# Optimization experiments

Hardware: AMD Instinct MI355X
Metric: run time of the kernel (lower is better)

The kernel has to match this reference:

```python
import jax, jax.numpy as jnp
import numpy as np

# Constructor constants (WindowCCC defaults)
STRIDE = 1
MAX_STRIDE = 125      # 25 * 5
WINDOW = 500          # 25 * 20


def setup_inputs() -> dict:
    key = jax.random.key(0)
    k1, k2 = jax.random.split(key)
    L = 16384000  # 32768 windows of 500
    return {
        "prediction": jax.random.normal(k1, (L,), dtype=jnp.float32),
        "ground_truth": jax.random.normal(k2, (L,), dtype=jnp.float32),
    }


def _suffix_sum(x):
    # suffix_sum[:, n] = sum_{i>=n} x[:, i]
    return jnp.cumsum(x[:, ::-1], axis=1)[:, ::-1]


def reference(prediction, ground_truth):
    # NOTE on faithfulness: in the torch source, `pred` is reassigned inside the
    # shift loop (drop first n, pad n zeros on top). Because shift indices are
    # strictly increasing (range(0, maxStride, stride)), the cumulative effect at
    # step n is exactly pred_n = [zeros(n), pred_orig[n:]]. We exploit that, and
    # express the per-shift mean/var/cov as suffix sums gathered at the shift
    # offsets -- one fused pass instead of O(num_wins * n_shifts) tiny kernels.
    W = WINDOW
    L = ground_truth.shape[0]
    num_wins = L // W
    g = ground_truth[: num_wins * W].reshape(num_wins, W)
    p = prediction[: num_wins * W].reshape(num_wins, W)

    shifts = jnp.arange(0, MAX_STRIDE, STRIDE)  # [S]
    Wf = jnp.asarray(W, p.dtype)

    # ground-truth stats (shift-independent), torch.var is unbiased (ddof=1)
    m_g = jnp.mean(g, axis=1, keepdims=True)                         # [nw,1]
    var_g = jnp.sum((g - m_g) ** 2, axis=1, keepdims=True) / (W - 1)  # [nw,1]

    # shifted-prediction stats via suffix sums, gathered at shift offsets
    Sp = _suffix_sum(p)[:, shifts]        # sum p_i, i>=n        [nw,S]
    Spp = _suffix_sum(p * p)[:, shifts]   # sum p_i^2, i>=n      [nw,S]
    Spg = _suffix_sum(p * g)[:, shifts]   # sum p_i g_i, i>=n    [nw,S]

    m_p = Sp / Wf                                   # mean of zero-padded pred_n
    var_p = (Spp - Wf * m_p * m_p) / (W - 1)        # unbiased var of pred_n
    cov = Spg / Wf - m_p * m_g                      # biased cov (torch.mean)

    denom = var_g + var_p + (m_g - m_p) ** 2
    ccc = 2.0 * cov / denom                          # [nw,S]

    cmin = jnp.min(ccc, axis=1)                      # [nw]
    return 1.0 - jnp.mean(cmin)
```

## Files before the change

kernel.cpp:

```cpp
#include <hip/hip_runtime.h>
#include <float.h>

#define WINDOW  500
#define NQUADS  125
#define NSHIFT  125
#define WPB     4

template <int CTRL, int RM>
__device__ __forceinline__ float dpp_add_step(float x) {
    int t = __builtin_amdgcn_update_dpp(0, __float_as_int(x), CTRL, RM, 0xf, false);
    return x + __int_as_float(t);
}
__device__ __forceinline__ float scan64_add(float x) {
    x = dpp_add_step<0x111, 0xf>(x);
    x = dpp_add_step<0x112, 0xf>(x);
    x = dpp_add_step<0x114, 0xf>(x);
    x = dpp_add_step<0x118, 0xf>(x);
    x = dpp_add_step<0x142, 0xa>(x);
    x = dpp_add_step<0x143, 0xc>(x);
    return x;
}
template <int CTRL, int RM>
__device__ __forceinline__ float dpp_min_step(float x) {
    int t = __builtin_amdgcn_update_dpp(0x7f800000 , __float_as_int(x),
                                        CTRL, RM, 0xf, false);
    return fminf(x, __int_as_float(t));
}
__device__ __forceinline__ float wave_min64(float x) {
    x = dpp_min_step<0x111, 0xf>(x);
    x = dpp_min_step<0x112, 0xf>(x);
    x = dpp_min_step<0x114, 0xf>(x);
    x = dpp_min_step<0x118, 0xf>(x);
    x = dpp_min_step<0x142, 0xa>(x);
    x = dpp_min_step<0x143, 0xc>(x);
    return __int_as_float(__builtin_amdgcn_readlane(__float_as_int(x), 63));
}
__device__ __forceinline__ float rl63(float x) {
    return __int_as_float(__builtin_amdgcn_readlane(__float_as_int(x), 63));
}
__device__ __forceinline__ float frcp(float x) {
    float r = __builtin_amdgcn_rcpf(x);
    return r * (2.0f - x * r);
}

__device__ __forceinline__ float ccc_eval(float Sp, float Spp, float Spg,
                                          float m_g, float var_g) {
    const float invW   = 1.0f / (float)WINDOW;
    const float invWm1 = 1.0f / (float)(WINDOW - 1);
    float m_p   = Sp * invW;
    float var_p = (Spp - (float)WINDOW * m_p * m_p) * invWm1;
    float cov   = Spg * invW - m_p * m_g;
    float d     = m_g - m_p;
    return 2.0f * cov * frcp(var_g + var_p + d * d);
}

template <bool TWO_STAGE>
__global__ __launch_bounds__(256) void window_ccc_kernel(
    const float4* __restrict__ pred4,
    const float4* __restrict__ gt4,
    float* __restrict__ block_out,
    int num_wins)
{
    __shared__ float s_cmin[WPB];
    const int wave = threadIdx.x >> 6;
    const int lane = threadIdx.x & 63;
    int w = blockIdx.x * WPB + wave;
    const bool valid = (w < num_wins);
    if (!valid) w = num_wins - 1;

    const float4* p4 = pred4 + (size_t)w * NQUADS;
    const float4* g4 = gt4   + (size_t)w * NQUADS;

    float4 pa = p4[lane];
    float4 ga = g4[lane];
    float4 pb = make_float4(0.f, 0.f, 0.f, 0.f);
    float4 gb = make_float4(0.f, 0.f, 0.f, 0.f);
    if (lane < NQUADS - 64) { pb = p4[64 + lane]; gb = g4[64 + lane]; }

    const float qp  = pa.x + pa.y + pa.z + pa.w;
    const float qpp = pa.x*pa.x + pa.y*pa.y + pa.z*pa.z + pa.w*pa.w;
    const float qpg = pa.x*ga.x + pa.y*ga.y + pa.z*ga.z + pa.w*ga.w;
    const float r1p  = pb.x + pb.y + pb.z + pb.w;
    const float r1pp = pb.x*pb.x + pb.y*pb.y + pb.z*pb.z + pb.w*pb.w;
    const float r1pg = pb.x*gb.x + pb.y*gb.y + pb.z*gb.z + pb.w*gb.w;
    const float lg  = ga.x + ga.y + ga.z + ga.w + gb.x + gb.y + gb.z + gb.w;
    const float lgg = ga.x*ga.x + ga.y*ga.y + ga.z*ga.z + ga.w*ga.w
                    + gb.x*gb.x + gb.y*gb.y + gb.z*gb.z + gb.w*gb.w;

    float c_p  = scan64_add(qp);
    float c_pp = scan64_add(qpp);
    float c_pg = scan64_add(qpg);
    float t1p  = scan64_add(r1p);
    float t1pp = scan64_add(r1pp);
    float t1pg = scan64_add(r1pg);
    float tg   = scan64_add(lg);
    float tgg  = scan64_add(lgg);

    const float sp  = rl63(c_p)  + rl63(t1p);
    const float spp = rl63(c_pp) + rl63(t1pp);
    const float spg = rl63(c_pg) + rl63(t1pg);
    const float sg  = rl63(tg);
    const float sgg = rl63(tgg);

    const float invW   = 1.0f / (float)WINDOW;
    const float invWm1 = 1.0f / (float)(WINDOW - 1);
    const float m_g   = sg * invW;
    const float var_g = (sgg - (float)WINDOW * m_g * m_g) * invWm1;

    float cmin = FLT_MAX;
    if (lane < 32) {
        float Sp  = sp  - (c_p  - qp);
        float Spp = spp - (c_pp - qpp);
        float Spg = spg - (c_pg - qpg);
        const int base = lane * 4;
        cmin = ccc_eval(Sp, Spp, Spg, m_g, var_g);
        Sp -= pa.x; Spp -= pa.x*pa.x; Spg -= pa.x*ga.x;
        if (base + 1 < NSHIFT) cmin = fminf(cmin, ccc_eval(Sp, Spp, Spg, m_g, var_g));
        Sp -= pa.y; Spp -= pa.y*pa.y; Spg -= pa.y*ga.y;
        if (base + 2 < NSHIFT) cmin = fminf(cmin, ccc_eval(Sp, Spp, Spg, m_g, var_g));
        Sp -= pa.z; Spp -= pa.z*pa.z; Spg -= pa.z*ga.z;
        if (base + 3 < NSHIFT) cmin = fminf(cmin, ccc_eval(Sp, Spp, Spg, m_g, var_g));
    }

    const float cm = wave_min64(cmin);

    if (lane == 0) s_cmin[wave] = valid ? cm : 0.f;
    __syncthreads();
    if (threadIdx.x == 0) {
        float s = s_cmin[0] + s_cmin[1] + s_cmin[2] + s_cmin[3];
        if (TWO_STAGE) block_out[blockIdx.x] = s;
        else           atomicAdd(block_out, s);
    }
}

__global__ __launch_bounds__(256) void window_ccc_finalize(
    const float* __restrict__ block_sums, int nblocks,
    float* __restrict__ out, int num_wins)
{
    float s = 0.f;
    for (int i = threadIdx.x; i < nblocks; i += 256) s += block_sums[i];
    #pragma unroll
    for (int off = 32; off >= 1; off >>= 1) s += __shfl_xor(s, off);
    __shared__ float ws[4];
    const int wave = threadIdx.x >> 6, lane = threadIdx.x & 63;
    if (lane == 0) ws[wave] = s;
    __syncthreads();
    if (threadIdx.x == 0)
        out[0] = 1.0f - (ws[0] + ws[1] + ws[2] + ws[3]) / (float)num_wins;
}

extern "C" void kernel_launch(void* const* d_in, const int* in_sizes, int n_in,
                              void* d_out, int out_size, void* d_ws, size_t ws_size,
                              hipStream_t stream) {
    const float4* pred4 = (const float4*)d_in[0];
    const float4* gt4   = (const float4*)d_in[1];
    float* out = (float*)d_out;
    float* ws  = (float*)d_ws;

    const int L = in_sizes[0];
    const int num_wins = L / WINDOW;
    const int nblocks  = (num_wins + WPB - 1) / WPB;

    if (ws_size >= (size_t)nblocks * sizeof(float)) {
        window_ccc_kernel<true><<<nblocks, 256, 0, stream>>>(pred4, gt4, ws, num_wins);
        window_ccc_finalize<<<1, 256, 0, stream>>>(ws, nblocks, out, num_wins);
    } else {
        hipMemsetAsync(ws, 0, sizeof(float), stream);
        window_ccc_kernel<false><<<nblocks, 256, 0, stream>>>(pred4, gt4, ws, num_wins);
        window_ccc_finalize<<<1, 256, 0, stream>>>(ws, 1, out, num_wins);
    }
}
```

Measured before the change: 34.23 us.

## Process four windows per wave with double-buffered register prefetch

Each wave now handles four windows strided across the grid instead of one, and the grid is cut by four. Loads for the next window are issued into a second register buffer before the current window is computed, so memory latency overlaps with the scans and CCC evaluation. A launch-bounds occupancy hint is added, and block partial sums and finalize work shrink. The trade-offs are higher register pressure and fewer blocks (2048) to fill the GPU.

```diff
diff --git a/kernel.cpp b/kernel.cpp
--- a/kernel.cpp
+++ b/kernel.cpp
@@ -5,6 +5,7 @@
 #define NQUADS  125
 #define NSHIFT  125
 #define WPB     4
+#define NWPW    4
 
 template <int CTRL, int RM>
 __device__ __forceinline__ float dpp_add_step(float x) {
@@ -22,8 +23,7 @@
 }
 template <int CTRL, int RM>
 __device__ __forceinline__ float dpp_min_step(float x) {
-    int t = __builtin_amdgcn_update_dpp(0x7f800000 , __float_as_int(x),
-                                        CTRL, RM, 0xf, false);
+    int t = __builtin_amdgcn_update_dpp(0x7f800000, __float_as_int(x), CTRL, RM, 0xf, false);
     return fminf(x, __int_as_float(t));
 }
 __device__ __forceinline__ float wave_min64(float x) {
@@ -54,28 +54,24 @@
     return 2.0f * cov * frcp(var_g + var_p + d * d);
 }
 
-template <bool TWO_STAGE>
-__global__ __launch_bounds__(256) void window_ccc_kernel(
-    const float4* __restrict__ pred4,
-    const float4* __restrict__ gt4,
-    float* __restrict__ block_out,
-    int num_wins)
+struct Win { float4 pa, ga, pb, gb; };
+
+__device__ __forceinline__ void load_win(const float4* __restrict__ pred4,
+                                         const float4* __restrict__ gt4,
+                                         int w, int lane, Win& d)
 {
-    __shared__ float s_cmin[WPB];
-    const int wave = threadIdx.x >> 6;
-    const int lane = threadIdx.x & 63;
-    int w = blockIdx.x * WPB + wave;
-    const bool valid = (w < num_wins);
-    if (!valid) w = num_wins - 1;
-
     const float4* p4 = pred4 + (size_t)w * NQUADS;
     const float4* g4 = gt4   + (size_t)w * NQUADS;
+    d.pa = p4[lane];
+    d.ga = g4[lane];
+    d.pb = make_float4(0.f, 0.f, 0.f, 0.f);
+    d.gb = make_float4(0.f, 0.f, 0.f, 0.f);
+    if (lane < NQUADS - 64) { d.pb = p4[64 + lane]; d.gb = g4[64 + lane]; }
+}
 
-    float4 pa = p4[lane];
-    float4 ga = g4[lane];
-    float4 pb = make_float4(0.f, 0.f, 0.f, 0.f);
-    float4 gb = make_float4(0.f, 0.f, 0.f, 0.f);
-    if (lane < NQUADS - 64) { pb = p4[64 + lane]; gb = g4[64 + lane]; }
+__device__ __forceinline__ float compute_win(const Win& d, int lane)
+{
+    const float4 pa = d.pa, ga = d.ga, pb = d.pb, gb = d.gb;
 
     const float qp  = pa.x + pa.y + pa.z + pa.w;
     const float qpp = pa.x*pa.x + pa.y*pa.y + pa.z*pa.z + pa.w*pa.w;
@@ -90,17 +86,11 @@
     float c_p  = scan64_add(qp);
     float c_pp = scan64_add(qpp);
     float c_pg = scan64_add(qpg);
-    float t1p  = scan64_add(r1p);
-    float t1pp = scan64_add(r1pp);
-    float t1pg = scan64_add(r1pg);
-    float tg   = scan64_add(lg);
-    float tgg  = scan64_add(lgg);
-
-    const float sp  = rl63(c_p)  + rl63(t1p);
-    const float spp = rl63(c_pp) + rl63(t1pp);
-    const float spg = rl63(c_pg) + rl63(t1pg);
-    const float sg  = rl63(tg);
-    const float sgg = rl63(tgg);
+    const float sp  = rl63(c_p)  + rl63(scan64_add(r1p));
+    const float spp = rl63(c_pp) + rl63(scan64_add(r1pp));
+    const float spg = rl63(c_pg) + rl63(scan64_add(r1pg));
+    const float sg  = rl63(scan64_add(lg));
+    const float sgg = rl63(scan64_add(lgg));
 
     const float invW   = 1.0f / (float)WINDOW;
     const float invWm1 = 1.0f / (float)(WINDOW - 1);
@@ -121,13 +111,45 @@
         Sp -= pa.z; Spp -= pa.z*pa.z; Spg -= pa.z*ga.z;
         if (base + 3 < NSHIFT) cmin = fminf(cmin, ccc_eval(Sp, Spp, Spg, m_g, var_g));
     }
+    return wave_min64(cmin);
+}
 
-    const float cm = wave_min64(cmin);
+template <bool TWO_STAGE>
+__global__ __launch_bounds__(256, 8) void window_ccc_kernel(
+    const float4* __restrict__ pred4,
+    const float4* __restrict__ gt4,
+    float* __restrict__ block_out,
+    int num_wins)
+{
+    __shared__ float s_sum[WPB];
+    const int wave   = threadIdx.x >> 6;
+    const int lane   = threadIdx.x & 63;
+    const int gwaves = gridDim.x * WPB;
+    const int gwave  = blockIdx.x * WPB + wave;
 
-    if (lane == 0) s_cmin[wave] = valid ? cm : 0.f;
+    const int  w0 = gwave;
+    const int  w1 = gwave + gwaves;
+    const int  w2 = gwave + 2 * gwaves;
+    const int  w3 = gwave + 3 * gwaves;
+    const bool v0 = (w0 < num_wins), v1 = (w1 < num_wins),
+               v2 = (w2 < num_wins), v3 = (w3 < num_wins);
+
+    Win A, B;
+    load_win(pred4, gt4, v0 ? w0 : 0, lane, A);
+    load_win(pred4, gt4, v1 ? w1 : 0, lane, B);
+
+    float ws = 0.f;
+    { float cm = compute_win(A, lane); if (v0) ws += cm; }
+    load_win(pred4, gt4, v2 ? w2 : 0, lane, A);
+    { float cm = compute_win(B, lane); if (v1) ws += cm; }
+    load_win(pred4, gt4, v3 ? w3 : 0, lane, B);
+    { float cm = compute_win(A, lane); if (v2) ws += cm; }
+    { float cm = compute_win(B, lane); if (v3) ws += cm; }
+
+    if (lane == 0) s_sum[wave] = ws;
     __syncthreads();
     if (threadIdx.x == 0) {
-        float s = s_cmin[0] + s_cmin[1] + s_cmin[2] + s_cmin[3];
+        float s = s_sum[0] + s_sum[1] + s_sum[2] + s_sum[3];
         if (TWO_STAGE) block_out[blockIdx.x] = s;
         else           atomicAdd(block_out, s);
     }
@@ -159,7 +181,8 @@
 
     const int L = in_sizes[0];
     const int num_wins = L / WINDOW;
-    const int nblocks  = (num_wins + WPB - 1) / WPB;
+    const int wins_per_block = WPB * NWPW;
+    const int nblocks = (num_wins + wins_per_block - 1) / wins_per_block;
 
     if (ws_size >= (size_t)nblocks * sizeof(float)) {
         window_ccc_kernel<true><<<nblocks, 256, 0, stream>>>(pred4, gt4, ws, num_wins);
```

Result: faster. 29.93 us (-12.6%).
